# Optimization experiments

Hardware: AMD Instinct MI355X
Metric: run time of the kernel (lower is better)

Reference implementation:

```python
import jax, jax.numpy as jnp
import numpy as np

C = 64  # channel dim fixed by Conv1D filters=64 and residual add

def setup_inputs() -> dict:
    key = jax.random.key(0)
    kF, kM, kN, kV = jax.random.split(key, 4)
    B, T = 8, 2048
    F = jax.random.normal(kF, (B, T, C), dtype=jnp.float32)
    # Conv1D(kernel_size=1, use_bias=False) == pointwise dense: weight [C_in, filters]
    scale = 1.0 / np.sqrt(C)
    W_M = jax.random.normal(kM, (C, C), dtype=jnp.float32) * scale
    W_N = jax.random.normal(kN, (C, C), dtype=jnp.float32) * scale
    W_V = jax.random.normal(kV, (C, C), dtype=jnp.float32) * scale
    return {"F": F, "W_M": W_M, "W_N": W_N, "W_V": W_V}

def reference(F, W_M, W_N, W_V):
    # 1x1 conv projections (pointwise matmul over channel dim)
    M = jnp.einsum('btc,cd->btd', F, W_M)  # Q
    N = jnp.einsum('btc,cd->btd', F, W_N)  # K
    V = jnp.einsum('btc,cd->btd', F, W_V)
    # correlation = Q @ K^T ; softmax over last axis (keras Softmax default)
    scores = jnp.einsum('bqd,bkd->bqk', M, N)  # [B, T, T]
    S = jax.nn.softmax(scores, axis=-1)
    out = jnp.einsum('bqk,bkd->bqd', S, V)
    return out + F  # residual
```

## Files before the change

### kernel.cpp

```cpp
#include <hip/hip_runtime.h>
#include <hip/hip_bf16.h>

#define B_ 8
#define T_ 2048
#define LOG2E 1.4426950408889634f

typedef _Float16 half8 __attribute__((ext_vector_type(8)));
typedef _Float16 half4 __attribute__((ext_vector_type(4)));
typedef float f32x4 __attribute__((ext_vector_type(4)));

#define MFMA16(A, Bv, Cv) __builtin_amdgcn_mfma_f32_16x16x32_f16((A), (Bv), (Cv), 0, 0, 0)

__device__ inline float xexp2(float x)
{
    float r;
    asm("v_exp_f32 %0, %1" : "=v"(r) : "v"(x));
    return r;
}

__global__ __launch_bounds__(256) void prepack_kernel(
    const float* __restrict__ WM, const float* __restrict__ WN,
    const float* __restrict__ WV, _Float16* __restrict__ Wp)
{
    const int idx = blockIdx.x * 256 + threadIdx.x;
    const int m = idx >> 12;
    const int r = idx & 4095;
    const int d = r >> 6;
    const int k = r & 63;
    const float* W = (m == 0) ? WM : (m == 1) ? WN : WV;
    Wp[m * 4096 + d * 64 + k] = (_Float16)W[k * 64 + d];
}

__global__ __launch_bounds__(256) void proj_kernel(
    const float* __restrict__ F, const _Float16* __restrict__ Wp,
    _Float16* __restrict__ Qh, _Float16* __restrict__ Kf,
    _Float16* __restrict__ Vf)
{
    const int lane = threadIdx.x & 63;
    const int dt   = threadIdx.x >> 6;
    const int ql = lane & 15;
    const int g  = lane >> 4;
    const int blk = blockIdx.x;
    const int b   = blk & 7;
    const int rt  = blk >> 3;
    const int rowbase = b * T_ + rt * 16;

    const float* fr = F + (size_t)(rowbase + ql) * 64;
    const f32x4 v00 = *(const f32x4*)(fr + 8 * g);
    const f32x4 v01 = *(const f32x4*)(fr + 8 * g + 4);
    const f32x4 v10 = *(const f32x4*)(fr + 32 + 8 * g);
    const f32x4 v11 = *(const f32x4*)(fr + 32 + 8 * g + 4);
    half8 af0, af1;
#pragma unroll
    for (int j = 0; j < 4; ++j) {
        af0[j]     = (_Float16)v00[j];
        af0[4 + j] = (_Float16)v01[j];
        af1[j]     = (_Float16)v10[j];
        af1[4 + j] = (_Float16)v11[j];
    }

    const half8* wq = (const half8*)(Wp);
    const half8* wk = (const half8*)(Wp + 4096);
    const half8* wv = (const half8*)(Wp + 8192);

    const int fi = (dt * 16 + ql) * 8;
    f32x4 z = {0.f, 0.f, 0.f, 0.f};
    f32x4 accQ = MFMA16(wq[fi + g], af0, z);
    accQ = MFMA16(wq[fi + 4 + g], af1, accQ);
    f32x4 accK = MFMA16(wk[fi + g], af0, z);
    accK = MFMA16(wk[fi + 4 + g], af1, accK);
    f32x4 accV = MFMA16(af0, wv[fi + g], z);
    accV = MFMA16(af1, wv[fi + 4 + g], accV);

    {
        half4 qs;
#pragma unroll
        for (int r = 0; r < 4; ++r) qs[r] = (_Float16)(accQ[r] * LOG2E);
        *(half4*)(Qh + (size_t)(rowbase + ql) * 64 + dt * 16 + 4 * g) = qs;
    }
    {
        half4 ks;
#pragma unroll
        for (int r = 0; r < 4; ++r) ks[r] = (_Float16)accK[r];
        const int d0 = dt * 16 + 4 * g;
        const int p  = ((d0 >> 5) << 2) | ((d0 >> 3) & 3);
        *(half4*)(Kf + (((size_t)b * 128 + rt) * 8 + p) * 128 + ql * 8 + (d0 & 7)) = ks;
    }
    {
        half4 vs;
#pragma unroll
        for (int r = 0; r < 4; ++r) vs[r] = (_Float16)accV[r];
        const int kt5 = rt >> 1;
        const int cp0 = 8 * g + 4 * (rt & 1);
        *(half4*)(Vf + ((((size_t)b * 64 + kt5) * 4 + dt) * 16 + ql) * 32 + cp0) = vs;
    }
}

#define PROC(qf0, qf1, a0, a1, a2, a3, mr, ls)                               \
    do {                                                                     \
        f32x4 s0 = {0.f, 0.f, 0.f, 0.f};                                     \
        f32x4 s1 = {0.f, 0.f, 0.f, 0.f};                                     \
        s0 = MFMA16(k0lo, qf0, s0);                                          \
        s0 = MFMA16(k0hi, qf1, s0);                                          \
        s1 = MFMA16(k1lo, qf0, s1);                                          \
        s1 = MFMA16(k1hi, qf1, s1);                                          \
        const float p0 = s0[0], p1 = s0[1], p2 = s0[2], p3 = s0[3];          \
        const float p4 = s1[0], p5 = s1[1], p6 = s1[2], p7 = s1[3];          \
        const float q0_ = fmaxf(fmaxf(p0, p1), p2);                          \
        const float q1_ = fmaxf(fmaxf(p3, p4), p5);                          \
        const float q2_ = fmaxf(fmaxf(p6, p7), q0_);                         \
        const float pm  = fmaxf(q1_, q2_);                                   \
        if (__any(pm - mr > 8.0f)) {                                         \
            float pmw = fmaxf(pm, __shfl_xor(pm, 16));                       \
            pmw = fmaxf(pmw, __shfl_xor(pmw, 32));                           \
            const float mnew = fmaxf(mr, pmw);                               \
            const float fac  = xexp2(mr - mnew);                             \
            mr = mnew;                                                       \
            ls *= fac;                                                       \
            const int lg = 4 * ((threadIdx.x & 63) >> 4);                    \
            const int lb = (threadIdx.x & 48);                               \
            const float f0 = __shfl(fac, lb | (lg + 0));                     \
            const float f1 = __shfl(fac, lb | (lg + 1));                     \
            const float f2 = __shfl(fac, lb | (lg + 2));                     \
            const float f3 = __shfl(fac, lb | (lg + 3));                     \
            a0[0] *= f0; a0[1] *= f1; a0[2] *= f2; a0[3] *= f3;              \
            a1[0] *= f0; a1[1] *= f1; a1[2] *= f2; a1[3] *= f3;              \
            a2[0] *= f0; a2[1] *= f1; a2[2] *= f2; a2[3] *= f3;              \
            a3[0] *= f0; a3[1] *= f1; a3[2] *= f2; a3[3] *= f3;              \
        }                                                                    \
        const float e0 = xexp2(p0 - mr), e1 = xexp2(p1 - mr);                \
        const float e2 = xexp2(p2 - mr), e3 = xexp2(p3 - mr);                \
        const float e4 = xexp2(p4 - mr), e5 = xexp2(p5 - mr);                \
        const float e6 = xexp2(p6 - mr), e7 = xexp2(p7 - mr);                \
        ls += ((e0 + e1) + (e2 + e3)) + ((e4 + e5) + (e6 + e7));             \
        half8 pav;                                                           \
        pav[0] = (_Float16)e0; pav[1] = (_Float16)e1;                        \
        pav[2] = (_Float16)e2; pav[3] = (_Float16)e3;                        \
        pav[4] = (_Float16)e4; pav[5] = (_Float16)e5;                        \
        pav[6] = (_Float16)e6; pav[7] = (_Float16)e7;                        \
        a0 = MFMA16(pav, v0, a0);                                            \
        a1 = MFMA16(pav, v1, a1);                                            \
        a2 = MFMA16(pav, v2, a2);                                            \
        a3 = MFMA16(pav, v3, a3);                                            \
    } while (0)

__global__ __launch_bounds__(512, 4) void attn_kernel(
    const _Float16* __restrict__ Qh, const _Float16* __restrict__ Kf,
    const _Float16* __restrict__ Vf, const float* __restrict__ F,
    float* __restrict__ out)
{
    __shared__ float Ol[4][64][68];
    __shared__ float Ml[4][64];
    __shared__ float Ll[4][64];

    const int lane = threadIdx.x & 63;
    const int wid  = threadIdx.x >> 6;
    const int tp   = wid & 1;
    const int ks   = wid >> 1;
    const int blk  = blockIdx.x;
    const int b    = blk & 7;
    const int tile = blk >> 3;
    const int ql = lane & 15;
    const int g  = lane >> 4;

    const _Float16* Qbb = Qh + (size_t)b * T_ * 64;
    const half8* KfB = (const half8*)Kf + (size_t)b * 16384;
    const half8* VfB = (const half8*)Vf + (size_t)b * 16384;

    const int qb = (tile << 6) + tp * 32;
    const half8* qpA = (const half8*)(Qbb + (qb +      ql) * 64);
    const half8* qpB = (const half8*)(Qbb + (qb + 16 + ql) * 64);
    const half8 qA0 = qpA[g], qA1 = qpA[4 + g];
    const half8 qB0 = qpB[g], qB1 = qpB[4 + g];

    const f32x4 z4 = {0.f, 0.f, 0.f, 0.f};
    f32x4 aA0 = z4, aA1 = z4, aA2 = z4, aA3 = z4;
    f32x4 aB0 = z4, aB1 = z4, aB2 = z4, aB3 = z4;
    float mA = -1e30f, lsA = 0.f;
    float mB = -1e30f, lsB = 0.f;

    const int kb0 = ks << 9;
    const half8* kA = KfB + (size_t)(kb0 >> 4) * 128 + g * 16 + ql;
    const half8* vA = VfB + (size_t)(kb0 >> 5) * 256 + ql * 4 + g;

    for (int it = 0; it < 16; ++it) {
        const half8 k0lo = kA[0];
        const half8 k0hi = kA[64];
        const half8 k1lo = kA[128];
        const half8 k1hi = kA[192];
        const half8 v0 = vA[0];
        const half8 v1 = vA[64];
        const half8 v2 = vA[128];
        const half8 v3 = vA[192];
        kA += 256;
        vA += 256;

        PROC(qA0, qA1, aA0, aA1, aA2, aA3, mA, lsA);
        PROC(qB0, qB1, aB0, aB1, aB2, aB3, mB, lsB);
    }

    lsA += __shfl_xor(lsA, 16); lsA += __shfl_xor(lsA, 32);
    lsB += __shfl_xor(lsB, 16); lsB += __shfl_xor(lsB, 32);

#pragma unroll
    for (int r = 0; r < 4; ++r) {
        Ol[ks][tp * 32 +      4 * g + r][ 0 + ql] = aA0[r];
        Ol[ks][tp * 32 +      4 * g + r][16 + ql] = aA1[r];
        Ol[ks][tp * 32 +      4 * g + r][32 + ql] = aA2[r];
        Ol[ks][tp * 32 +      4 * g + r][48 + ql] = aA3[r];
        Ol[ks][tp * 32 + 16 + 4 * g + r][ 0 + ql] = aB0[r];
        Ol[ks][tp * 32 + 16 + 4 * g + r][16 + ql] = aB1[r];
        Ol[ks][tp * 32 + 16 + 4 * g + r][32 + ql] = aB2[r];
        Ol[ks][tp * 32 + 16 + 4 * g + r][48 + ql] = aB3[r];
    }
    if (g == 0) {
        Ml[ks][tp * 32 +      ql] = mA;  Ll[ks][tp * 32 +      ql] = lsA;
        Ml[ks][tp * 32 + 16 + ql] = mB;  Ll[ks][tp * 32 + 16 + ql] = lsB;
    }
    __syncthreads();

    const int tid = threadIdx.x;
    const int qq  = tid >> 3;
    const int d0  = (tid & 7) * 8;

    float mm[4], lv[4];
#pragma unroll
    for (int s = 0; s < 4; ++s) {
        mm[s] = Ml[s][qq];
        lv[s] = Ll[s][qq];
    }
    const float ms = fmaxf(fmaxf(mm[0], mm[1]), fmaxf(mm[2], mm[3]));
    float lt = 0.f;
    f32x4 oa = {0.f, 0.f, 0.f, 0.f};
    f32x4 ob2 = {0.f, 0.f, 0.f, 0.f};
#pragma unroll
    for (int s = 0; s < 4; ++s) {
        const float sc = xexp2(mm[s] - ms);
        lt += lv[s] * sc;
        oa  += *(const f32x4*)(&Ol[s][qq][d0])     * sc;
        ob2 += *(const f32x4*)(&Ol[s][qq][d0 + 4]) * sc;
    }
    const float inv = 1.0f / lt;
    const size_t grow = (size_t)b * T_ + (tile << 6) + qq;
    const f32x4 fr0 = *(const f32x4*)(F + grow * 64 + d0);
    const f32x4 fr1 = *(const f32x4*)(F + grow * 64 + d0 + 4);
    *(f32x4*)(out + grow * 64 + d0)     = oa * inv + fr0;
    *(f32x4*)(out + grow * 64 + d0 + 4) = ob2 * inv + fr1;
}

extern "C" void kernel_launch(void* const* d_in, const int* in_sizes, int n_in,
                              void* d_out, int out_size, void* d_ws, size_t ws_size,
                              hipStream_t stream)
{
    const float* F  = (const float*)d_in[0];
    const float* WM = (const float*)d_in[1];
    const float* WN = (const float*)d_in[2];
    const float* WV = (const float*)d_in[3];
    float* out = (float*)d_out;

    const size_t proj_bytes = (size_t)B_ * T_ * 64 * sizeof(_Float16);
    char* ws = (char*)d_ws;
    _Float16* Qh = (_Float16*)(ws);
    _Float16* Kf = (_Float16*)(ws + proj_bytes);
    _Float16* Vf = (_Float16*)(ws + 2 * proj_bytes);
    _Float16* Wp = (_Float16*)(ws + 3 * proj_bytes);

    hipLaunchKernelGGL(prepack_kernel, dim3(48), dim3(256), 0, stream,
                       WM, WN, WV, Wp);
    hipLaunchKernelGGL(proj_kernel, dim3(B_ * T_ / 16), dim3(256), 0, stream,
                       F, Wp, Qh, Kf, Vf);
    hipLaunchKernelGGL(attn_kernel, dim3(B_ * T_ / 64), dim3(512), 0, stream,
                       Qh, Kf, Vf, F, out);
}
```

Baseline: 32.52 us.

## Halve attention block to 32 queries and prefetch next K/V tile in registers

The attention kernel now uses 256-thread blocks covering 32 query rows, with four waves each taking a quarter of the key range, and launches twice as many blocks. The K/V loop loads the next iteration's fragments before running the current softmax and MFMA work, which is meant to hide global-load latency. This doubles the number of blocks and the total K/V reads, and the extra prefetch registers can lower occupancy.

```diff
diff --git a/kernel.cpp b/kernel.cpp
--- a/kernel.cpp
+++ b/kernel.cpp
@@ -144,19 +144,17 @@
         a3 = MFMA16(pav, v3, a3);                                            \
     } while (0)
 
-__global__ __launch_bounds__(512, 4) void attn_kernel(
+__global__ __launch_bounds__(256, 2) void attn_kernel(
     const _Float16* __restrict__ Qh, const _Float16* __restrict__ Kf,
     const _Float16* __restrict__ Vf, const float* __restrict__ F,
     float* __restrict__ out)
 {
-    __shared__ float Ol[4][64][68];
-    __shared__ float Ml[4][64];
-    __shared__ float Ll[4][64];
+    __shared__ float Ol[4][32][68];
+    __shared__ float Ml[4][32];
+    __shared__ float Ll[4][32];
 
     const int lane = threadIdx.x & 63;
     const int wid  = threadIdx.x >> 6;
-    const int tp   = wid & 1;
-    const int ks   = wid >> 1;
     const int blk  = blockIdx.x;
     const int b    = blk & 7;
     const int tile = blk >> 3;
@@ -167,7 +165,7 @@
     const half8* KfB = (const half8*)Kf + (size_t)b * 16384;
     const half8* VfB = (const half8*)Vf + (size_t)b * 16384;
 
-    const int qb = (tile << 6) + tp * 32;
+    const int qb = tile * 32;
     const half8* qpA = (const half8*)(Qbb + (qb +      ql) * 64);
     const half8* qpB = (const half8*)(Qbb + (qb + 16 + ql) * 64);
     const half8 qA0 = qpA[g], qA1 = qpA[4 + g];
@@ -179,24 +177,41 @@
     float mA = -1e30f, lsA = 0.f;
     float mB = -1e30f, lsB = 0.f;
 
-    const int kb0 = ks << 9;
+    const int kb0 = wid << 9;
     const half8* kA = KfB + (size_t)(kb0 >> 4) * 128 + g * 16 + ql;
     const half8* vA = VfB + (size_t)(kb0 >> 5) * 256 + ql * 4 + g;
 
+    half8 k0lo = kA[0];
+    half8 k0hi = kA[64];
+    half8 k1lo = kA[128];
+    half8 k1hi = kA[192];
+    half8 v0 = vA[0];
+    half8 v1 = vA[64];
+    half8 v2 = vA[128];
+    half8 v3 = vA[192];
+
     for (int it = 0; it < 16; ++it) {
-        const half8 k0lo = kA[0];
-        const half8 k0hi = kA[64];
-        const half8 k1lo = kA[128];
-        const half8 k1hi = kA[192];
-        const half8 v0 = vA[0];
-        const half8 v1 = vA[64];
-        const half8 v2 = vA[128];
-        const half8 v3 = vA[192];
+        half8 nk0lo, nk0hi, nk1lo, nk1hi, nv0, nv1, nv2, nv3;
+        if (it < 15) {
+            nk0lo = kA[256];
+            nk0hi = kA[256 + 64];
+            nk1lo = kA[256 + 128];
+            nk1hi = kA[256 + 192];
+            nv0 = vA[256];
+            nv1 = vA[256 + 64];
+            nv2 = vA[256 + 128];
+            nv3 = vA[256 + 192];
+        }
+
+        PROC(qA0, qA1, aA0, aA1, aA2, aA3, mA, lsA);
+        PROC(qB0, qB1, aB0, aB1, aB2, aB3, mB, lsB);
+
+        if (it < 15) {
+            k0lo = nk0lo; k0hi = nk0hi; k1lo = nk1lo; k1hi = nk1hi;
+            v0 = nv0; v1 = nv1; v2 = nv2; v3 = nv3;
+        }
         kA += 256;
         vA += 256;
-
-        PROC(qA0, qA1, aA0, aA1, aA2, aA3, mA, lsA);
-        PROC(qB0, qB1, aB0, aB1, aB2, aB3, mB, lsB);
     }
 
     lsA += __shfl_xor(lsA, 16); lsA += __shfl_xor(lsA, 32);
@@ -204,18 +219,18 @@
 
 #pragma unroll
     for (int r = 0; r < 4; ++r) {
-        Ol[ks][tp * 32 +      4 * g + r][ 0 + ql] = aA0[r];
-        Ol[ks][tp * 32 +      4 * g + r][16 + ql] = aA1[r];
-        Ol[ks][tp * 32 +      4 * g + r][32 + ql] = aA2[r];
-        Ol[ks][tp * 32 +      4 * g + r][48 + ql] = aA3[r];
-        Ol[ks][tp * 32 + 16 + 4 * g + r][ 0 + ql] = aB0[r];
-        Ol[ks][tp * 32 + 16 + 4 * g + r][16 + ql] = aB1[r];
-        Ol[ks][tp * 32 + 16 + 4 * g + r][32 + ql] = aB2[r];
-        Ol[ks][tp * 32 + 16 + 4 * g + r][48 + ql] = aB3[r];
+        Ol[wid][     4 * g + r][ 0 + ql] = aA0[r];
+        Ol[wid][     4 * g + r][16 + ql] = aA1[r];
+        Ol[wid][     4 * g + r][32 + ql] = aA2[r];
+        Ol[wid][     4 * g + r][48 + ql] = aA3[r];
+        Ol[wid][16 + 4 * g + r][ 0 + ql] = aB0[r];
+        Ol[wid][16 + 4 * g + r][16 + ql] = aB1[r];
+        Ol[wid][16 + 4 * g + r][32 + ql] = aB2[r];
+        Ol[wid][16 + 4 * g + r][48 + ql] = aB3[r];
     }
     if (g == 0) {
-        Ml[ks][tp * 32 +      ql] = mA;  Ll[ks][tp * 32 +      ql] = lsA;
-        Ml[ks][tp * 32 + 16 + ql] = mB;  Ll[ks][tp * 32 + 16 + ql] = lsB;
+        Ml[wid][     ql] = mA;  Ll[wid][     ql] = lsA;
+        Ml[wid][16 + ql] = mB;  Ll[wid][16 + ql] = lsB;
     }
     __syncthreads();
 
@@ -241,7 +256,7 @@
         ob2 += *(const f32x4*)(&Ol[s][qq][d0 + 4]) * sc;
     }
     const float inv = 1.0f / lt;
-    const size_t grow = (size_t)b * T_ + (tile << 6) + qq;
+    const size_t grow = (size_t)b * T_ + qb + qq;
     const f32x4 fr0 = *(const f32x4*)(F + grow * 64 + d0);
     const f32x4 fr1 = *(const f32x4*)(F + grow * 64 + d0 + 4);
     *(f32x4*)(out + grow * 64 + d0)     = oa * inv + fr0;
@@ -269,6 +284,6 @@
                        WM, WN, WV, Wp);
     hipLaunchKernelGGL(proj_kernel, dim3(B_ * T_ / 16), dim3(256), 0, stream,
                        F, Wp, Qh, Kf, Vf);
-    hipLaunchKernelGGL(attn_kernel, dim3(B_ * T_ / 64), dim3(512), 0, stream,
+    hipLaunchKernelGGL(attn_kernel, dim3(B_ * T_ / 32), dim3(256), 0, stream,
                        Qh, Kf, Vf, F, out);
 }
```

Result: no change. 32.22 us (-0.9%).
